# Performance work log

Hardware: AMD Instinct MI355X
Metric: run time of the kernel (lower is better)

Reference implementation:

```python
import jax, jax.numpy as jnp
import numpy as np

N = 50000
E = 1_600_000
H = 128
L = 6
GF = 10
NUM_GRAPHS = 1
EPS = 1e-5
MSG_IN = H + GF + 3 + 2 * (6 + 1)   # 155
UPD_IN = H + H + GF                  # 266
EMB_IN = GF + 1 + 6                  # 17
OUT_F = 9
MAC_F = 4


def _mlp2_relu(x, W1, b1, W2, b2):
    # Linear->ReLU->Linear->ReLU
    return jax.nn.relu(jax.nn.relu(x @ W1 + b1) @ W2 + b2)


def setup_inputs() -> dict:
    key = jax.random.key(0)
    ks = jax.random.split(key, 40)
    s = 0.05
    inp = {
        "v": jax.random.normal(ks[0], (N, 6), jnp.float32),
        "pos": jax.random.uniform(ks[1], (N, 3), jnp.float32),
        "r": jax.random.uniform(ks[2], (N, 1), jnp.float32),
        "domain": jnp.ones((3,), jnp.float32),
        "t": jax.random.uniform(ks[3], (2,), jnp.float32),
        "domain_next": jnp.ones((3,), jnp.float32),
        "t_next": jax.random.uniform(ks[4], (2,), jnp.float32),
        "edge_index": jax.random.randint(ks[5], (2, E), 0, N, jnp.int32),
        "batch": jnp.zeros((N,), jnp.int32),
        # embedding MLP
        "emb_W1": jax.random.normal(ks[6], (EMB_IN, H), jnp.float32) * s,
        "emb_b1": jnp.zeros((H,), jnp.float32),
        "emb_W2": jax.random.normal(ks[7], (H, H), jnp.float32) * s,
        "emb_b2": jnp.zeros((H,), jnp.float32),
        # stacked per-layer GNN params
        "msg_W1": jax.random.normal(ks[8], (L, MSG_IN, H), jnp.float32) * s,
        "msg_b1": jnp.zeros((L, H), jnp.float32),
        "msg_W2": jax.random.normal(ks[9], (L, H, H), jnp.float32) * s,
        "msg_b2": jnp.zeros((L, H), jnp.float32),
        "upd_W1": jax.random.normal(ks[10], (L, UPD_IN, H), jnp.float32) * s,
        "upd_b1": jnp.zeros((L, H), jnp.float32),
        "upd_W2": jax.random.normal(ks[11], (L, H, H), jnp.float32) * s,
        "upd_b2": jnp.zeros((L, H), jnp.float32),
        # output heads
        "out_W1": jax.random.normal(ks[12], (H, H), jnp.float32) * s,
        "out_b1": jnp.zeros((H,), jnp.float32),
        "out_W2": jax.random.normal(ks[13], (H, OUT_F), jnp.float32) * s,
        "out_b2": jnp.zeros((OUT_F,), jnp.float32),
        "mac_W1": jax.random.normal(ks[14], (H, H), jnp.float32) * s,
        "mac_b1": jnp.zeros((H,), jnp.float32),
        "mac_W2": jax.random.normal(ks[15], (H, MAC_F), jnp.float32) * s,
        "mac_b2": jnp.zeros((MAC_F,), jnp.float32),
    }
    return inp


def reference(v, pos, r, domain, t, domain_next, t_next, edge_index, batch,
              emb_W1, emb_b1, emb_W2, emb_b2,
              msg_W1, msg_b1, msg_W2, msg_b2,
              upd_W1, upd_b1, upd_W2, upd_b2,
              out_W1, out_b1, out_W2, out_b2,
              mac_W1, mac_b1, mac_W2, mac_b2):
    n = v.shape[0]
    gf = jnp.concatenate([domain, t, domain_next, t_next])      # [10]
    gf_n = jnp.broadcast_to(gf, (n, gf.shape[0]))
    node_features = jnp.concatenate([pos, v], axis=1)           # [N,9]

    x0 = jnp.concatenate([r, v, gf_n], axis=1)                  # [N,17]
    h = _mlp2_relu(x0, emb_W1, emb_b1, emb_W2, emb_b2)          # [N,128]

    src = edge_index[0]  # x_j (source)
    dst = edge_index[1]  # x_i (target, aggregation index)
    e = src.shape[0]
    gf_e = jnp.broadcast_to(gf, (e, gf.shape[0]))
    deg = jax.ops.segment_sum(jnp.ones((e,), h.dtype), dst, num_segments=n)
    deg = jnp.maximum(deg, 1.0)[:, None]
    cnt = jax.ops.segment_sum(jnp.ones((n,), h.dtype), batch, num_segments=NUM_GRAPHS)[:, None]

    for l in range(msg_W1.shape[0]):
        # edge message: gather-concat-MLP
        m_in = jnp.concatenate(
            [h[dst] - h[src], v[dst], v[src], r[dst], r[src],
             pos[dst] - pos[src], gf_e], axis=1)                 # [E,155]
        m = _mlp2_relu(m_in, msg_W1[l], msg_b1[l], msg_W2[l], msg_b2[l])
        agg = jax.ops.segment_sum(m, dst, num_segments=n) / deg # mean aggregate
        # node update (residual since in==out)
        u_in = jnp.concatenate([h, agg, gf_n], axis=1)           # [N,266]
        h = h + _mlp2_relu(u_in, upd_W1[l], upd_b1[l], upd_W2[l], upd_b2[l])
        # InstanceNorm per graph (no affine, biased variance)
        mean = jax.ops.segment_sum(h, batch, num_segments=NUM_GRAPHS) / cnt
        var = jax.ops.segment_sum(h * h, batch, num_segments=NUM_GRAPHS) / cnt - mean * mean
        h = (h - mean[batch]) * jax.lax.rsqrt(var[batch] + EPS)

    pred = jax.nn.relu(h @ out_W1 + out_b1) @ out_W2 + out_b2 + node_features
    pred_x = jnp.remainder(pred[:, :3], domain_next)
    pred_v = pred[:, 3:]

    h_mean = jax.ops.segment_sum(h, batch, num_segments=NUM_GRAPHS) / cnt
    pred_macro = (jax.nn.relu(h_mean @ mac_W1 + mac_b1) @ mac_W2 + mac_b2)[0]
    return pred_x, pred_v, pred_macro
```

## Files before the change

kernel.cpp:

```cpp
#include <hip/hip_runtime.h>

#define NN 50000
#define NE 1600000
#define HD 128
#define NL 6
#define EPSV 1e-5f
#define UPD_OFF 442368

typedef _Float16 h8 __attribute__((ext_vector_type(8)));
typedef float f4 __attribute__((ext_vector_type(4)));

__global__ void k_prep(const float* __restrict__ dom, const float* __restrict__ t,
                       const float* __restrict__ domn, const float* __restrict__ tn,
                       float* __restrict__ gf) {
  int i = threadIdx.x;
  if (i < 3) gf[i] = dom[i];
  if (i < 2) gf[3 + i] = t[i];
  if (i < 3) gf[5 + i] = domn[i];
  if (i < 2) gf[8 + i] = tn[i];
}

__global__ void k_initnorm(float* __restrict__ mean, float* __restrict__ rsig) {
  int f = threadIdx.x;
  mean[f] = 0.f; rsig[f] = 1.f;
}

__global__ void k_stats(const float* __restrict__ colsum, const float* __restrict__ colsumsq,
                        float* __restrict__ mean, float* __restrict__ rsig) {
  int f = threadIdx.x;
  float m = colsum[f] * (1.f / (float)NN);
  float var = colsumsq[f] * (1.f / (float)NN) - m * m;
  mean[f] = m;
  rsig[f] = rsqrtf(var + EPSV);
}

__global__ void k_bias(const float* __restrict__ gf,
                       const float* __restrict__ msgW1, const float* __restrict__ msgb1,
                       const float* __restrict__ updW1, const float* __restrict__ updb1,
                       const float* __restrict__ embW1, const float* __restrict__ embb1,
                       float* __restrict__ beff) {
  int s = blockIdx.x, f = threadIdx.x;
  float acc;
  if (s < 6) {
    acc = msgb1[s * HD + f];
    const float* W = msgW1 + (size_t)s * 155 * HD;
    for (int g = 0; g < 10; g++) acc += gf[g] * W[(145 + g) * HD + f];
  } else if (s < 12) {
    int l = s - 6;
    acc = updb1[l * HD + f];
    const float* W = updW1 + (size_t)l * 266 * HD;
    for (int g = 0; g < 10; g++) acc += gf[g] * W[(256 + g) * HD + f];
  } else {
    acc = embb1[f];
    for (int g = 0; g < 10; g++) acc += gf[g] * embW1[(7 + g) * HD + f];
  }
  beff[s * HD + f] = acc;
}

__global__ void k_wpack(const float* __restrict__ msgW1, const float* __restrict__ msgW2,
                        const float* __restrict__ updW1, const float* __restrict__ updW2,
                        _Float16* __restrict__ wpack) {
  int b = blockIdx.x;
  int nt = b & 7;
  int rest = b >> 3;
  int part = rest % 21;
  int layer = rest / 21;
  int lane = threadIdx.x;
  int g = lane >> 4, c = lane & 15;
  const float* W; int Ksrc, ks; size_t base;
  if (part < 5)       { W = msgW1 + (size_t)layer * 155 * HD; Ksrc = 145; ks = part;
                        base = (size_t)layer * 73728 + (size_t)(ks * 8 + nt) * 1024; }
  else if (part < 9)  { W = msgW2 + (size_t)layer * HD * HD;  Ksrc = 128; ks = part - 5;
                        base = (size_t)layer * 73728 + (size_t)(40 + ks * 8 + nt) * 1024; }
  else if (part < 17) { W = updW1 + (size_t)layer * 266 * HD; Ksrc = 256; ks = part - 9;
                        base = UPD_OFF + (size_t)layer * 98304 + (size_t)(ks * 8 + nt) * 1024; }
  else                { W = updW2 + (size_t)layer * HD * HD;  Ksrc = 128; ks = part - 17;
                        base = UPD_OFF + (size_t)layer * 98304 + (size_t)(64 + ks * 8 + nt) * 1024; }
  h8 hv, lv;
#pragma unroll
  for (int j = 0; j < 8; j++) {
    int k = ks * 32 + 8 * g + j;
    float w = (k < Ksrc) ? W[(size_t)k * HD + nt * 16 + c] : 0.f;
    _Float16 hi = (_Float16)w;
    hv[j] = hi;
    lv[j] = (_Float16)(w - (float)hi);
  }
  _Float16* bp = wpack + base;
  *(h8*)(bp + lane * 8) = hv;
  *(h8*)(bp + 512 + lane * 8) = lv;
}

__global__ void k_degi(const int* __restrict__ dst, int* __restrict__ degi) {
  int i = blockIdx.x * blockDim.x + threadIdx.x;
  int stride = gridDim.x * blockDim.x;
  for (; i < NE; i += stride) atomicAdd(&degi[dst[i]], 1);
}

__global__ void k_deginv(const int* __restrict__ degi, float* __restrict__ deginv) {
  int i = blockIdx.x * blockDim.x + threadIdx.x;
  if (i < NN) deginv[i] = 1.0f / (float)max(degi[i], 1);
}

__global__ __launch_bounds__(1024) void k_scan(const int* __restrict__ degi,
                                               int* __restrict__ cursor) {
  __shared__ int ps[1024];
  int t = threadIdx.x;
  const int CH = 49;
  int lo = t * CH, hi = min(lo + CH, NN);
  int s = 0;
  for (int i = lo; i < hi; i++) s += degi[i];
  ps[t] = s;
  __syncthreads();
  for (int d = 1; d < 1024; d <<= 1) {
    int vv = (t >= d) ? ps[t - d] : 0;
    __syncthreads();
    ps[t] += vv;
    __syncthreads();
  }
  int base = (t > 0) ? ps[t - 1] : 0;
  for (int i = lo; i < hi; i++) { cursor[i] = base; base += degi[i]; }
}

__global__ void k_scatter(const int* __restrict__ src, const int* __restrict__ dst,
                          int* __restrict__ cursor, unsigned long long* __restrict__ es8) {
  int i = blockIdx.x * blockDim.x + threadIdx.x;
  int stride = gridDim.x * blockDim.x;
  for (; i < NE; i += stride) {
    int d = dst[i];
    int p = atomicAdd(&cursor[d], 1);
    es8[p] = ((unsigned long long)(unsigned)d << 32) | (unsigned)src[i];
  }
}

__global__ __launch_bounds__(256) void k_embed(
    const float* __restrict__ v, const float* __restrict__ r,
    const float* __restrict__ W1, const float* __restrict__ b1eff,
    const float* __restrict__ W2, const float* __restrict__ b2,
    float* __restrict__ h) {
  __shared__ float sIn[16][8];
  __shared__ float sW[32][128];
  __shared__ float sH[16][132];
  int tid = threadIdx.x;
  int n0 = blockIdx.x * 16;
  int tx = tid & 63, ty = tid >> 6;
  if (tid < 16 * 7) {
    int n = tid / 7, k = tid - n * 7;
    int gi = n0 + n;
    sIn[n][k] = (k == 0) ? r[gi] : v[gi * 6 + k - 1];
  }
  for (int idx = tid; idx < 7 * 128; idx += 256) sW[idx >> 7][idx & 127] = W1[idx];
  __syncthreads();
  float acc0[4], acc1[4];
  float bb0 = b1eff[tx], bb1 = b1eff[tx + 64];
#pragma unroll
  for (int i = 0; i < 4; i++) { acc0[i] = bb0; acc1[i] = bb1; }
  for (int k = 0; k < 7; k++) {
    float w0 = sW[k][tx], w1 = sW[k][tx + 64];
#pragma unroll
    for (int i = 0; i < 4; i++) {
      float a = sIn[ty * 4 + i][k];
      acc0[i] += a * w0; acc1[i] += a * w1;
    }
  }
  __syncthreads();
#pragma unroll
  for (int i = 0; i < 4; i++) {
    sH[ty * 4 + i][tx] = fmaxf(acc0[i], 0.f);
    sH[ty * 4 + i][tx + 64] = fmaxf(acc1[i], 0.f);
  }
  float bc0 = b2[tx], bc1 = b2[tx + 64];
#pragma unroll
  for (int i = 0; i < 4; i++) { acc0[i] = bc0; acc1[i] = bc1; }
  for (int k0 = 0; k0 < 128; k0 += 32) {
    __syncthreads();
    for (int idx = tid; idx < 32 * 128; idx += 256)
      sW[idx >> 7][idx & 127] = W2[(k0 + (idx >> 7)) * 128 + (idx & 127)];
    __syncthreads();
    for (int kk = 0; kk < 32; kk++) {
      float w0 = sW[kk][tx], w1 = sW[kk][tx + 64];
#pragma unroll
      for (int i = 0; i < 4; i++) {
        float a = sH[ty * 4 + i][k0 + kk];
        acc0[i] += a * w0; acc1[i] += a * w1;
      }
    }
  }
  for (int i = 0; i < 4; i++) {
    int gi = n0 + ty * 4 + i;
    h[gi * 128 + tx] = fmaxf(acc0[i], 0.f);
    h[gi * 128 + tx + 64] = fmaxf(acc1[i], 0.f);
  }
}

__global__ __launch_bounds__(512) void k_uv(
    const float* __restrict__ h, const float* __restrict__ v, const float* __restrict__ r,
    const float* __restrict__ pos,
    const _Float16* __restrict__ wl, const float* __restrict__ W1,
    const float* __restrict__ b1eff,
    const float* __restrict__ mean, const float* __restrict__ rsig,
    float* __restrict__ U, float* __restrict__ Vv) {
  __shared__ char smem[32768];
  __shared__ float sW1s[17][128];
  __shared__ float sNode[64][10];
  __shared__ float sMean[128], sRsig[128];
  int tid = threadIdx.x;
  int lane = tid & 63;
  int wid = __builtin_amdgcn_readfirstlane(tid >> 6);
  int n0 = blockIdx.x * 64;

  if (tid < 128) { sMean[tid] = mean[tid]; sRsig[tid] = rsig[tid]; }
  for (int idx = tid; idx < 17 * 128; idx += 512)
    sW1s[idx >> 7][idx & 127] = W1[(128 + (idx >> 7)) * HD + (idx & 127)];
  for (int idx = tid; idx < 640; idx += 512) {
    int n = idx / 10, j = idx - n * 10;
    int gn = n0 + n;
    float val = 0.f;
    if (gn < NN) val = (j < 6) ? v[gn * 6 + j] : (j == 6) ? r[gn] : pos[gn * 3 + (j - 7)];
    sNode[n][j] = val;
  }
  __syncthreads();
#pragma unroll
  for (int it = 0; it < 2; it++) {
    int idx = tid + it * 512;
    int n = idx >> 4, kg = idx & 15;
    int gn = n0 + n;
    float4 a0 = {0,0,0,0}, a1 = {0,0,0,0};
    if (gn < NN) {
      const float4* hp = (const float4*)(h + (size_t)gn * 128 + kg * 8);
      a0 = hp[0]; a1 = hp[1];
    }
    int kb = kg * 8;
    h8 hv, lv;
#define SPLH(s, x, kkk) { float pv = ((x) - sMean[kkk]) * sRsig[kkk]; _Float16 hh = (_Float16)pv; hv[s] = hh; lv[s] = (_Float16)(pv - (float)hh); }
    SPLH(0, a0.x, kb+0) SPLH(1, a0.y, kb+1) SPLH(2, a0.z, kb+2) SPLH(3, a0.w, kb+3)
    SPLH(4, a1.x, kb+4) SPLH(5, a1.y, kb+5) SPLH(6, a1.z, kb+6) SPLH(7, a1.w, kb+7)
#undef SPLH
    int byteoff = (n * 256 + kg * 16) ^ ((n & 7) << 4);
    *(h8*)(smem + byteoff) = hv;
    *(h8*)(smem + 16384 + byteoff) = lv;
  }
  __syncthreads();

  h8 w1hi[4], w1lo[4];
#pragma unroll
  for (int ks = 0; ks < 4; ks++) {
    const _Float16* p = wl + (size_t)(ks * 8 + wid) * 1024 + lane * 8;
    w1hi[ks] = *(const h8*)p;
    w1lo[ks] = *(const h8*)(p + 512);
  }
  int arow = lane & 15, g4 = lane >> 4;
  f4 acc[4];
#pragma unroll
  for (int mt = 0; mt < 4; mt++) acc[mt] = (f4){0.f, 0.f, 0.f, 0.f};
#pragma unroll
  for (int ks = 0; ks < 4; ks++) {
#pragma unroll
    for (int mt = 0; mt < 4; mt++) {
      int row = mt * 16 + arow;
      int byte = (row * 256 + ks * 64 + g4 * 16) ^ ((row & 7) << 4);
      h8 ahi = *(const h8*)(smem + byte);
      h8 alo = *(const h8*)(smem + 16384 + byte);
      acc[mt] = __builtin_amdgcn_mfma_f32_16x16x32_f16(ahi, w1hi[ks], acc[mt], 0, 0, 0);
      acc[mt] = __builtin_amdgcn_mfma_f32_16x16x32_f16(ahi, w1lo[ks], acc[mt], 0, 0, 0);
      acc[mt] = __builtin_amdgcn_mfma_f32_16x16x32_f16(alo, w1hi[ks], acc[mt], 0, 0, 0);
    }
  }
  int cc = wid * 16 + arow;
  float b1v = b1eff[cc];
#pragma unroll
  for (int mt = 0; mt < 4; mt++) {
#pragma unroll
    for (int i = 0; i < 4; i++) {
      int n = mt * 16 + 4 * g4 + i;
      int gn = n0 + n;
      if (gn < NN) {
        float P = acc[mt][i];
        float qd = b1v, qs = 0.f;
#pragma unroll
        for (int j = 0; j < 6; j++) {
          float nv = sNode[n][j];
          qd += nv * sW1s[j][cc];
          qs += nv * sW1s[6 + j][cc];
        }
        float nr = sNode[n][6];
        qd += nr * sW1s[12][cc];
        qs += nr * sW1s[13][cc];
#pragma unroll
        for (int j = 0; j < 3; j++) {
          float pq = sNode[n][7 + j] * sW1s[14 + j][cc];
          qd += pq; qs -= pq;
        }
        U[(size_t)gn * 128 + cc] = P + qd;
        Vv[(size_t)gn * 128 + cc] = qs - P;
      }
    }
  }
}

__global__ __launch_bounds__(512) void k_msg3(
    const float* __restrict__ U, const float* __restrict__ Vv,
    const unsigned long long* __restrict__ es8,
    const _Float16* __restrict__ wl, const float* __restrict__ b2,
    float* __restrict__ agg) {
  __shared__ char smem[33792];
  __shared__ int sSrcA[64], sDstA[64];
  float* sM = (float*)smem;
  int tid = threadIdx.x;
  int lane = tid & 63;
  int wid = __builtin_amdgcn_readfirstlane(tid >> 6);
  size_t e0 = (size_t)blockIdx.x * 64;

  if (tid < 64) {
    unsigned long long w = es8[e0 + tid];
    sSrcA[tid] = (int)(w & 0xffffffffULL);
    sDstA[tid] = (int)(w >> 32);
  }
  h8 w2hi[4], w2lo[4];
#pragma unroll
  for (int ks = 0; ks < 4; ks++) {
    const _Float16* p = wl + (size_t)(40 + ks * 8 + wid) * 1024 + lane * 8;
    w2hi[ks] = *(const h8*)p;
    w2lo[ks] = *(const h8*)(p + 512);
  }
  __syncthreads();

#pragma unroll
  for (int it = 0; it < 2; it++) {
    int c = tid + it * 512;
    int e = c >> 4, kg = c & 15;
    int dd = sDstA[e], ss = sSrcA[e];
    const float4* up = (const float4*)(U + (size_t)dd * 128 + kg * 8);
    const float4* vp = (const float4*)(Vv + (size_t)ss * 128 + kg * 8);
    float4 u0 = up[0], u1 = up[1];
    float4 v0 = vp[0], v1 = vp[1];
    h8 hv, lv;
#define SPL(s, x) { float pre = fmaxf((x), 0.f); _Float16 hh = (_Float16)pre; hv[s] = hh; lv[s] = (_Float16)(pre - (float)hh); }
    SPL(0, u0.x + v0.x) SPL(1, u0.y + v0.y) SPL(2, u0.z + v0.z) SPL(3, u0.w + v0.w)
    SPL(4, u1.x + v1.x) SPL(5, u1.y + v1.y) SPL(6, u1.z + v1.z) SPL(7, u1.w + v1.w)
#undef SPL
    int byteoff = (e * 256 + kg * 16) ^ ((e & 7) << 4);
    *(h8*)(smem + byteoff) = hv;
    *(h8*)(smem + 16384 + byteoff) = lv;
  }
  __syncthreads();

  int arow = lane & 15, g4 = lane >> 4;
  float b2v = b2[wid * 16 + arow];
  f4 acc[4];
#pragma unroll
  for (int mt = 0; mt < 4; mt++) acc[mt] = (f4){b2v, b2v, b2v, b2v};
#pragma unroll
  for (int ks = 0; ks < 4; ks++) {
#pragma unroll
    for (int mt = 0; mt < 4; mt++) {
      int row = mt * 16 + arow;
      int byte = (row * 256 + ks * 64 + g4 * 16) ^ ((row & 7) << 4);
      h8 ahi = *(const h8*)(smem + byte);
      h8 alo = *(const h8*)(smem + 16384 + byte);
      acc[mt] = __builtin_amdgcn_mfma_f32_16x16x32_f16(ahi, w2hi[ks], acc[mt], 0, 0, 0);
      acc[mt] = __builtin_amdgcn_mfma_f32_16x16x32_f16(ahi, w2lo[ks], acc[mt], 0, 0, 0);
      acc[mt] = __builtin_amdgcn_mfma_f32_16x16x32_f16(alo, w2hi[ks], acc[mt], 0, 0, 0);
    }
  }
  __syncthreads();
  int colc = wid * 16 + arow;
#pragma unroll
  for (int mt = 0; mt < 4; mt++)
#pragma unroll
    for (int i = 0; i < 4; i++) {
      int row = mt * 16 + 4 * g4 + i;
      sM[row * 132 + colc] = fmaxf(acc[mt][i], 0.f);
    }
  __syncthreads();

  int f = tid & 127, g = tid >> 7;
  float racc = 0.f;
  int prev = -1;
  for (int e = g * 16; e < g * 16 + 16; e++) {
    int d = sDstA[e];
    if (d != prev) {
      if (prev >= 0) atomicAdd(&agg[(size_t)prev * 128 + f], racc);
      racc = 0.f;
      prev = d;
    }
    racc += sM[e * 132 + f];
  }
  atomicAdd(&agg[(size_t)prev * 128 + f], racc);
}

__global__ __launch_bounds__(512) void k_upd2(
    float* __restrict__ h, const float* __restrict__ agg, const float* __restrict__ deginv,
    const _Float16* __restrict__ wl, const float* __restrict__ b1eff,
    const float* __restrict__ b2,
    const float* __restrict__ mean, const float* __restrict__ rsig,
    float* __restrict__ colsum, float* __restrict__ colsumsq) {
  __shared__ char smem[65536];
  __shared__ float sMean[128], sRsig[128];
  int tid = threadIdx.x;
  int lane = tid & 63;
  int wid = __builtin_amdgcn_readfirstlane(tid >> 6);
  int n0 = blockIdx.x * 64;
  if (tid < 128) { sMean[tid] = mean[tid]; sRsig[tid] = rsig[tid]; }
  __syncthreads();
#pragma unroll
  for (int it = 0; it < 4; it++) {
    int c = tid + it * 512;
    int n = c >> 5, kg = c & 31;
    int gn = n0 + n;
    h8 hv, lv;
    if (gn < NN) {
      if (kg < 16) {
        const float4* hp = (const float4*)(h + (size_t)gn * 128 + kg * 8);
        float4 a0 = hp[0], a1 = hp[1];
        int kb = kg * 8;
#define SPLH(s, x, kkk) { float pv = ((x) - sMean[kkk]) * sRsig[kkk]; _Float16 hh = (_Float16)pv; hv[s] = hh; lv[s] = (_Float16)(pv - (float)hh); }
        SPLH(0, a0.x, kb+0) SPLH(1, a0.y, kb+1) SPLH(2, a0.z, kb+2) SPLH(3, a0.w, kb+3)
        SPLH(4, a1.x, kb+4) SPLH(5, a1.y, kb+5) SPLH(6, a1.z, kb+6) SPLH(7, a1.w, kb+7)
#undef SPLH
      } else {
        float dg = deginv[gn];
        const float4* ap = (const float4*)(agg + (size_t)gn * 128 + (kg - 16) * 8);
        float4 a0 = ap[0], a1 = ap[1];
#define SPLA(s, x) { float pv = (x) * dg; _Float16 hh = (_Float16)pv; hv[s] = hh; lv[s] = (_Float16)(pv - (float)hh); }
        SPLA(0, a0.x) SPLA(1, a0.y) SPLA(2, a0.z) SPLA(3, a0.w)
        SPLA(4, a1.x) SPLA(5, a1.y) SPLA(6, a1.z) SPLA(7, a1.w)
#undef SPLA
      }
    } else {
#pragma unroll
      for (int j = 0; j < 8; j++) { hv[j] = (_Float16)0.f; lv[j] = (_Float16)0.f; }
    }
    int byteoff = (n * 512 + kg * 16) ^ ((n & 7) << 4);
    *(h8*)(smem + byteoff) = hv;
    *(h8*)(smem + 32768 + byteoff) = lv;
  }
  __syncthreads();

  int arow = lane & 15, g4 = lane >> 4;
  int colc = wid * 16 + arow;
  float b1v = b1eff[colc];
  f4 acc[4];
#pragma unroll
  for (int mt = 0; mt < 4; mt++) acc[mt] = (f4){b1v, b1v, b1v, b1v};
#pragma unroll
  for (int ksb = 0; ksb < 2; ksb++) {
    h8 whi[4], wlo[4];
#pragma unroll
    for (int kk = 0; kk < 4; kk++) {
      const _Float16* p = wl + (size_t)((ksb * 4 + kk) * 8 + wid) * 1024 + lane * 8;
      whi[kk] = *(const h8*)p;
      wlo[kk] = *(const h8*)(p + 512);
    }
#pragma unroll
    for (int kk = 0; kk < 4; kk++) {
#pragma unroll
      for (int mt = 0; mt < 4; mt++) {
        int row = mt * 16 + arow;
        int byte = (row * 512 + (ksb * 4 + kk) * 64 + g4 * 16) ^ ((row & 7) << 4);
        h8 ahi = *(const h8*)(smem + byte);
        h8 alo = *(const h8*)(smem + 32768 + byte);
        acc[mt] = __builtin_amdgcn_mfma_f32_16x16x32_f16(ahi, whi[kk], acc[mt], 0, 0, 0);
        acc[mt] = __builtin_amdgcn_mfma_f32_16x16x32_f16(ahi, wlo[kk], acc[mt], 0, 0, 0);
        acc[mt] = __builtin_amdgcn_mfma_f32_16x16x32_f16(alo, whi[kk], acc[mt], 0, 0, 0);
      }
    }
  }
  __syncthreads();
#pragma unroll
  for (int mt = 0; mt < 4; mt++)
#pragma unroll
    for (int i = 0; i < 4; i++) {
      int row = mt * 16 + 4 * g4 + i;
      int byte = (row * 256 + colc * 2) ^ ((row & 7) << 4);
      float hvf = fmaxf(acc[mt][i], 0.f);
      _Float16 hh = (_Float16)hvf;
      *(_Float16*)(smem + byte) = hh;
      *(_Float16*)(smem + 16384 + byte) = (_Float16)(hvf - (float)hh);
    }
  __syncthreads();
  float b2v = b2[colc];
  f4 acc2[4];
#pragma unroll
  for (int mt = 0; mt < 4; mt++) acc2[mt] = (f4){b2v, b2v, b2v, b2v};
  {
    h8 whi[4], wlo[4];
#pragma unroll
    for (int kk = 0; kk < 4; kk++) {
      const _Float16* p = wl + (size_t)(64 + kk * 8 + wid) * 1024 + lane * 8;
      whi[kk] = *(const h8*)p;
      wlo[kk] = *(const h8*)(p + 512);
    }
#pragma unroll
    for (int kk = 0; kk < 4; kk++) {
#pragma unroll
      for (int mt = 0; mt < 4; mt++) {
        int row = mt * 16 + arow;
        int byte = (row * 256 + kk * 64 + g4 * 16) ^ ((row & 7) << 4);
        h8 ahi = *(const h8*)(smem + byte);
        h8 alo = *(const h8*)(smem + 16384 + byte);
        acc2[mt] = __builtin_amdgcn_mfma_f32_16x16x32_f16(ahi, whi[kk], acc2[mt], 0, 0, 0);
        acc2[mt] = __builtin_amdgcn_mfma_f32_16x16x32_f16(ahi, wlo[kk], acc2[mt], 0, 0, 0);
        acc2[mt] = __builtin_amdgcn_mfma_f32_16x16x32_f16(alo, whi[kk], acc2[mt], 0, 0, 0);
      }
    }
  }
  float s = 0.f, q = 0.f;
  float mc = sMean[colc], rc = sRsig[colc];
#pragma unroll
  for (int mt = 0; mt < 4; mt++) {
#pragma unroll
    for (int i = 0; i < 4; i++) {
      int row = mt * 16 + 4 * g4 + i;
      int gn = n0 + row;
      if (gn < NN) {
        float hraw = h[(size_t)gn * 128 + colc];
        float hn = (hraw - mc) * rc;
        float hv = hn + fmaxf(acc2[mt][i], 0.f);
        h[(size_t)gn * 128 + colc] = hv;
        s += hv; q += hv * hv;
      }
    }
  }
  __syncthreads();
  float* red = (float*)(smem + 32768);
  red[(colc * 4 + g4) * 2 + 0] = s;
  red[(colc * 4 + g4) * 2 + 1] = q;
  __syncthreads();
  if (tid < 128) {
    float ss = 0.f, qq = 0.f;
#pragma unroll
    for (int g = 0; g < 4; g++) { ss += red[(tid * 4 + g) * 2]; qq += red[(tid * 4 + g) * 2 + 1]; }
    atomicAdd(&colsum[tid], ss);
    atomicAdd(&colsumsq[tid], qq);
  }
}

__global__ __launch_bounds__(256) void k_out(
    const float* __restrict__ h, const float* __restrict__ pos, const float* __restrict__ v,
    const float* __restrict__ gf,
    const float* __restrict__ mean, const float* __restrict__ rsig,
    const float* __restrict__ W1, const float* __restrict__ b1,
    const float* __restrict__ W2, const float* __restrict__ b2,
    float* __restrict__ out) {
  __shared__ float sH[16][132];
  __shared__ float sW[32][128];
  __shared__ float sMean[128], sRsig[128];
  int tid = threadIdx.x;
  int n0 = blockIdx.x * 16;
  int tx = tid & 63, ty = tid >> 6;
  if (tid < 128) { sMean[tid] = mean[tid]; sRsig[tid] = rsig[tid]; }
  __syncthreads();
  for (int idx = tid; idx < 16 * 128; idx += 256) {
    int n = idx >> 7, k = idx & 127;
    sH[n][k] = (h[(size_t)(n0 + n) * 128 + k] - sMean[k]) * sRsig[k];
  }
  float acc0[4], acc1[4];
  float bb0 = b1[tx], bb1 = b1[tx + 64];
#pragma unroll
  for (int i = 0; i < 4; i++) { acc0[i] = bb0; acc1[i] = bb1; }
  for (int k0 = 0; k0 < 128; k0 += 32) {
    __syncthreads();
    for (int idx = tid; idx < 32 * 128; idx += 256)
      sW[idx >> 7][idx & 127] = W1[(k0 + (idx >> 7)) * 128 + (idx & 127)];
    __syncthreads();
    for (int kk = 0; kk < 32; kk++) {
      float w0 = sW[kk][tx], w1 = sW[kk][tx + 64];
#pragma unroll
      for (int i = 0; i < 4; i++) {
        float a = sH[ty * 4 + i][k0 + kk];
        acc0[i] += a * w0; acc1[i] += a * w1;
      }
    }
  }
  __syncthreads();
#pragma unroll
  for (int i = 0; i < 4; i++) {
    sH[ty * 4 + i][tx] = fmaxf(acc0[i], 0.f);
    sH[ty * 4 + i][tx + 64] = fmaxf(acc1[i], 0.f);
  }
  __syncthreads();
  if (tid < 144) {
    int n = tid / 9, j = tid - n * 9;
    float a = b2[j];
    for (int k = 0; k < 128; k++) a += sH[n][k] * W2[k * 9 + j];
    int gi = n0 + n;
    if (j < 3) {
      float p = a + pos[gi * 3 + j];
      float d = gf[5 + j];
      float m = fmodf(p, d);
      if (m < 0.f) m += d;
      out[(size_t)gi * 3 + j] = m;
    } else {
      float p = a + v[gi * 6 + (j - 3)];
      out[(size_t)NN * 3 + (size_t)gi * 6 + (j - 3)] = p;
    }
  }
}

__global__ void k_macro(const float* __restrict__ b1,
                        const float* __restrict__ W2, const float* __restrict__ b2,
                        float* __restrict__ out) {
  __shared__ float hid[128];
  int f = threadIdx.x;
  hid[f] = fmaxf(b1[f], 0.f);
  __syncthreads();
  if (f < 4) {
    float a = b2[f];
    for (int k = 0; k < 128; k++) a += hid[k] * W2[k * 4 + f];
    out[(size_t)NN * 9 + f] = a;
  }
}

extern "C" void kernel_launch(void* const* d_in, const int* in_sizes, int n_in,
                              void* d_out, int out_size, void* d_ws, size_t ws_size,
                              hipStream_t stream) {
  (void)in_sizes; (void)n_in; (void)out_size; (void)ws_size;
  const float* v    = (const float*)d_in[0];
  const float* pos  = (const float*)d_in[1];
  const float* r    = (const float*)d_in[2];
  const float* dom  = (const float*)d_in[3];
  const float* t    = (const float*)d_in[4];
  const float* domn = (const float*)d_in[5];
  const float* tn   = (const float*)d_in[6];
  const int*   eidx = (const int*)d_in[7];
  const float* embW1 = (const float*)d_in[9];
  const float* embb1 = (const float*)d_in[10];
  const float* embW2 = (const float*)d_in[11];
  const float* embb2 = (const float*)d_in[12];
  const float* msgW1 = (const float*)d_in[13];
  const float* msgb1 = (const float*)d_in[14];
  const float* msgW2 = (const float*)d_in[15];
  const float* msgb2 = (const float*)d_in[16];
  const float* updW1 = (const float*)d_in[17];
  const float* updb1 = (const float*)d_in[18];
  const float* updW2 = (const float*)d_in[19];
  const float* updb2 = (const float*)d_in[20];
  const float* outW1 = (const float*)d_in[21];
  const float* outb1 = (const float*)d_in[22];
  const float* outW2 = (const float*)d_in[23];
  const float* outb2 = (const float*)d_in[24];
  const float* macb1 = (const float*)d_in[26];
  const float* macW2 = (const float*)d_in[27];
  const float* macb2 = (const float*)d_in[28];

  const int* srcp = eidx;
  const int* dstp = eidx + NE;

  char* ws = (char*)d_ws;
  float* h        = (float*)(ws);
  float* agg      = (float*)(ws + 25600000);
  float* U        = (float*)(ws + 51200000);
  float* Vv       = (float*)(ws + 76800000);
  unsigned long long* es8 = (unsigned long long*)(ws + 102400000);
  int*   degi     = (int*)(ws + 115200000);
  float* deginv   = (float*)(ws + 115400000);
  int*   cursor   = (int*)(ws + 115600000);
  float* gf       = (float*)(ws + 115800000);
  float* beff     = (float*)(ws + 115800064);
  float* colsum   = (float*)(ws + 115806720);
  float* colsumsq = (float*)(ws + 115807232);
  float* meanb    = (float*)(ws + 115807744);
  float* rsigb    = (float*)(ws + 115808256);
  _Float16* wpack = (_Float16*)(ws + 115808768);
  float* outp     = (float*)d_out;

  k_prep<<<1, 64, 0, stream>>>(dom, t, domn, tn, gf);
  k_bias<<<13, 128, 0, stream>>>(gf, msgW1, msgb1, updW1, updb1, embW1, embb1, beff);
  k_wpack<<<1008, 64, 0, stream>>>(msgW1, msgW2, updW1, updW2, wpack);
  k_initnorm<<<1, 128, 0, stream>>>(meanb, rsigb);

  hipMemsetAsync(degi, 0, NN * sizeof(int), stream);
  k_degi<<<4096, 256, 0, stream>>>(dstp, degi);
  k_deginv<<<(NN + 255) / 256, 256, 0, stream>>>(degi, deginv);
  k_scan<<<1, 1024, 0, stream>>>(degi, cursor);
  k_scatter<<<6250, 256, 0, stream>>>(srcp, dstp, cursor, es8);

  k_embed<<<NN / 16, 256, 0, stream>>>(v, r, embW1, beff + 12 * HD, embW2, embb2, h);

  for (int l = 0; l < NL; l++) {
    k_uv<<<(NN + 63) / 64, 512, 0, stream>>>(h, v, r, pos,
                                             wpack + (size_t)l * 73728,
                                             msgW1 + (size_t)l * 155 * HD,
                                             beff + l * HD, meanb, rsigb, U, Vv);
    hipMemsetAsync(agg, 0, (size_t)NN * 128 * sizeof(float), stream);
    hipMemsetAsync(colsum, 0, 1024, stream);
    k_msg3<<<NE / 64, 512, 0, stream>>>(U, Vv, es8,
                                        wpack + (size_t)l * 73728,
                                        msgb2 + l * HD, agg);
    k_upd2<<<(NN + 63) / 64, 512, 0, stream>>>(h, agg, deginv,
                                               wpack + UPD_OFF + (size_t)l * 98304,
                                               beff + (6 + l) * HD, updb2 + l * HD,
                                               meanb, rsigb, colsum, colsumsq);
    k_stats<<<1, 128, 0, stream>>>(colsum, colsumsq, meanb, rsigb);
  }

  k_out<<<NN / 16, 256, 0, stream>>>(h, pos, v, gf, meanb, rsigb,
                                     outW1, outb1, outW2, outb2, outp);
  k_macro<<<1, 128, 0, stream>>>(macb1, macW2, macb2, outp);
}
```

Before: 2.164 ms.

## Restructure message kernel to per-wave edge tiles without shared memory

Rewrites the edge message kernel so each wave independently gathers 16 edges' U/V rows directly into MFMA A-fragments in registers, computes all 128 output columns, and reduces by destination in registers before atomics. This removes shared-memory staging and block barriers and shrinks the block to 256 threads. In exchange it reloads W2 fragments from global memory per wave and reduces over only 4 edges per lane group, increasing the number of atomic adds to the aggregate buffer.

```diff
diff --git a/kernel.cpp b/kernel.cpp
--- a/kernel.cpp
+++ b/kernel.cpp
@@ -297,95 +297,81 @@
   }
 }
 
-__global__ __launch_bounds__(512) void k_msg3(
+__global__ __launch_bounds__(256) void k_msg4(
     const float* __restrict__ U, const float* __restrict__ Vv,
     const unsigned long long* __restrict__ es8,
     const _Float16* __restrict__ wl, const float* __restrict__ b2,
     float* __restrict__ agg) {
-  __shared__ char smem[33792];
-  __shared__ int sSrcA[64], sDstA[64];
-  float* sM = (float*)smem;
   int tid = threadIdx.x;
   int lane = tid & 63;
-  int wid = __builtin_amdgcn_readfirstlane(tid >> 6);
-  size_t e0 = (size_t)blockIdx.x * 64;
-
-  if (tid < 64) {
-    unsigned long long w = es8[e0 + tid];
-    sSrcA[tid] = (int)(w & 0xffffffffULL);
-    sDstA[tid] = (int)(w >> 32);
-  }
-  h8 w2hi[4], w2lo[4];
+  int wid = tid >> 6;
+  size_t eb = (size_t)blockIdx.x * 64 + (size_t)wid * 16;
+  int arow = lane & 15, g4 = lane >> 4;
+
+  unsigned long long wA = es8[eb + arow];
+  const float* Up = U + (size_t)(unsigned)(wA >> 32) * 128;
+  const float* Vp = Vv + (size_t)(unsigned)(wA & 0xffffffffULL) * 128;
+
+  int dOut[4];
+#pragma unroll
+  for (int i = 0; i < 4; i++)
+    dOut[i] = (int)(es8[eb + 4 * g4 + i] >> 32);
+
+  h8 ahi[4], alo[4];
 #pragma unroll
   for (int ks = 0; ks < 4; ks++) {
-    const _Float16* p = wl + (size_t)(40 + ks * 8 + wid) * 1024 + lane * 8;
-    w2hi[ks] = *(const h8*)p;
-    w2lo[ks] = *(const h8*)(p + 512);
-  }
-  __syncthreads();
-
-#pragma unroll
-  for (int it = 0; it < 2; it++) {
-    int c = tid + it * 512;
-    int e = c >> 4, kg = c & 15;
-    int dd = sDstA[e], ss = sSrcA[e];
-    const float4* up = (const float4*)(U + (size_t)dd * 128 + kg * 8);
-    const float4* vp = (const float4*)(Vv + (size_t)ss * 128 + kg * 8);
-    float4 u0 = up[0], u1 = up[1];
-    float4 v0 = vp[0], v1 = vp[1];
+    int off = ks * 32 + g4 * 8;
+    float4 u0 = *(const float4*)(Up + off);
+    float4 u1 = *(const float4*)(Up + off + 4);
+    float4 v0 = *(const float4*)(Vp + off);
+    float4 v1 = *(const float4*)(Vp + off + 4);
     h8 hv, lv;
 #define SPL(s, x) { float pre = fmaxf((x), 0.f); _Float16 hh = (_Float16)pre; hv[s] = hh; lv[s] = (_Float16)(pre - (float)hh); }
     SPL(0, u0.x + v0.x) SPL(1, u0.y + v0.y) SPL(2, u0.z + v0.z) SPL(3, u0.w + v0.w)
     SPL(4, u1.x + v1.x) SPL(5, u1.y + v1.y) SPL(6, u1.z + v1.z) SPL(7, u1.w + v1.w)
 #undef SPL
-    int byteoff = (e * 256 + kg * 16) ^ ((e & 7) << 4);
-    *(h8*)(smem + byteoff) = hv;
-    *(h8*)(smem + 16384 + byteoff) = lv;
-  }
-  __syncthreads();
-
-  int arow = lane & 15, g4 = lane >> 4;
-  float b2v = b2[wid * 16 + arow];
-  f4 acc[4];
-#pragma unroll
-  for (int mt = 0; mt < 4; mt++) acc[mt] = (f4){b2v, b2v, b2v, b2v};
-#pragma unroll
-  for (int ks = 0; ks < 4; ks++) {
-#pragma unroll
-    for (int mt = 0; mt < 4; mt++) {
-      int row = mt * 16 + arow;
-      int byte = (row * 256 + ks * 64 + g4 * 16) ^ ((row & 7) << 4);
-      h8 ahi = *(const h8*)(smem + byte);
-      h8 alo = *(const h8*)(smem + 16384 + byte);
-      acc[mt] = __builtin_amdgcn_mfma_f32_16x16x32_f16(ahi, w2hi[ks], acc[mt], 0, 0, 0);
-      acc[mt] = __builtin_amdgcn_mfma_f32_16x16x32_f16(ahi, w2lo[ks], acc[mt], 0, 0, 0);
-      acc[mt] = __builtin_amdgcn_mfma_f32_16x16x32_f16(alo, w2hi[ks], acc[mt], 0, 0, 0);
-    }
-  }
-  __syncthreads();
-  int colc = wid * 16 + arow;
-#pragma unroll
-  for (int mt = 0; mt < 4; mt++)
-#pragma unroll
-    for (int i = 0; i < 4; i++) {
-      int row = mt * 16 + 4 * g4 + i;
-      sM[row * 132 + colc] = fmaxf(acc[mt][i], 0.f);
-    }
-  __syncthreads();
-
-  int f = tid & 127, g = tid >> 7;
-  float racc = 0.f;
+    ahi[ks] = hv; alo[ks] = lv;
+  }
+
+  f4 acc[8];
+#pragma unroll
+  for (int nt = 0; nt < 8; nt++) {
+    float b2v = b2[nt * 16 + arow];
+    f4 a = (f4){b2v, b2v, b2v, b2v};
+#pragma unroll
+    for (int ks = 0; ks < 4; ks++) {
+      const _Float16* p = wl + (size_t)(40 + ks * 8 + nt) * 1024 + lane * 8;
+      h8 whi = *(const h8*)p;
+      h8 wlo = *(const h8*)(p + 512);
+      a = __builtin_amdgcn_mfma_f32_16x16x32_f16(ahi[ks], whi, a, 0, 0, 0);
+      a = __builtin_amdgcn_mfma_f32_16x16x32_f16(ahi[ks], wlo, a, 0, 0, 0);
+      a = __builtin_amdgcn_mfma_f32_16x16x32_f16(alo[ks], whi, a, 0, 0, 0);
+    }
+    acc[nt] = a;
+  }
+
+  float racc[8];
   int prev = -1;
-  for (int e = g * 16; e < g * 16 + 16; e++) {
-    int d = sDstA[e];
+#pragma unroll
+  for (int i = 0; i < 4; i++) {
+    int d = dOut[i];
     if (d != prev) {
-      if (prev >= 0) atomicAdd(&agg[(size_t)prev * 128 + f], racc);
-      racc = 0.f;
+      if (prev >= 0) {
+#pragma unroll
+        for (int nt = 0; nt < 8; nt++)
+          atomicAdd(&agg[(size_t)prev * 128 + nt * 16 + arow], racc[nt]);
+      }
+#pragma unroll
+      for (int nt = 0; nt < 8; nt++) racc[nt] = fmaxf(acc[nt][i], 0.f);
       prev = d;
-    }
-    racc += sM[e * 132 + f];
-  }
-  atomicAdd(&agg[(size_t)prev * 128 + f], racc);
+    } else {
+#pragma unroll
+      for (int nt = 0; nt < 8; nt++) racc[nt] += fmaxf(acc[nt][i], 0.f);
+    }
+  }
+#pragma unroll
+  for (int nt = 0; nt < 8; nt++)
+    atomicAdd(&agg[(size_t)prev * 128 + nt * 16 + arow], racc[nt]);
 }
 
 __global__ __launch_bounds__(512) void k_upd2(
@@ -684,7 +670,7 @@
                                              beff + l * HD, meanb, rsigb, U, Vv);
     hipMemsetAsync(agg, 0, (size_t)NN * 128 * sizeof(float), stream);
     hipMemsetAsync(colsum, 0, 1024, stream);
-    k_msg3<<<NE / 64, 512, 0, stream>>>(U, Vv, es8,
+    k_msg4<<<NE / 64, 256, 0, stream>>>(U, Vv, es8,
                                         wpack + (size_t)l * 73728,
                                         msgb2 + l * HD, agg);
     k_upd2<<<(NN + 63) / 64, 512, 0, stream>>>(h, agg, deginv,
```

After: 5.490 ms. +153.7%, slower.
